# Kernel optimization log

Hardware: AMD Instinct MI355X
Metric: run time of the kernel (lower is better)

Reference implementation:

```python
import jax, jax.numpy as jnp
import numpy as np

LOC_SIZE, CID_SIZE, UID_SIZE, TIM_SIZE = 10000, 300, 1000, 48
LOC_EMB, CID_EMB, UID_EMB, TIM_EMB = 256, 64, 64, 32
HID, ENC_HID = 500, 250            # hidden_size, history_hidden_size
SEQ, TGT = 2048, 256
INPUT = LOC_EMB + TIM_EMB + CID_EMB  # 352


def setup_inputs() -> dict:
    key = jax.random.key(0)
    ks = jax.random.split(key, 32)
    n = lambda i, shape, s=0.05: (jax.random.normal(ks[i], shape, dtype=jnp.float32) * s)
    d = {}
    d["loc"] = jax.random.randint(ks[0], (SEQ, 1), 0, LOC_SIZE)
    d["tim"] = jax.random.randint(ks[1], (SEQ, 1), 0, TIM_SIZE)
    d["cid"] = jax.random.randint(ks[2], (SEQ, 1), 0, CID_SIZE)
    d["uid"] = jax.random.randint(ks[3], (1,), 0, UID_SIZE)
    d["target"] = jax.random.randint(ks[4], (TGT, 1), 0, LOC_SIZE)
    d["target_len"] = TGT
    d["time_sim_matrix"] = jax.random.uniform(ks[5], (TIM_SIZE, TIM_SIZE), dtype=jnp.float32)
    # keep distances away from 0 since the model computes 1/dist
    d["poi_distance_matrix"] = jax.random.uniform(ks[6], (LOC_SIZE, LOC_SIZE), dtype=jnp.float32, minval=0.1, maxval=2.0)
    d["poi_cid_tim"] = jax.random.uniform(ks[7], (TIM_SIZE, CID_SIZE), dtype=jnp.float32)
    # embedding tables (emb_loc/emb_cid are pretrained+frozen in the original)
    d["weight"] = n(8, (LOC_SIZE, LOC_EMB))
    d["weight_cid"] = n(9, (CID_SIZE, CID_EMB))
    d["emb_uid_w"] = n(10, (UID_SIZE, UID_EMB))
    d["emb_tim_w"] = n(11, (TIM_SIZE, TIM_EMB))
    # bidirectional encoder LSTM (hidden 250), gate order i,f,g,o like torch
    d["enc_Wih_f"] = n(12, (4 * ENC_HID, INPUT))
    d["enc_Whh_f"] = n(13, (4 * ENC_HID, ENC_HID))
    d["enc_b_f"] = jnp.zeros((4 * ENC_HID,), jnp.float32)
    d["enc_Wih_b"] = n(14, (4 * ENC_HID, INPUT))
    d["enc_Whh_b"] = n(15, (4 * ENC_HID, ENC_HID))
    d["enc_b_b"] = jnp.zeros((4 * ENC_HID,), jnp.float32)
    # decoder LSTM (hidden 500)
    d["dec_Wih"] = n(16, (4 * HID, INPUT))
    d["dec_Whh"] = n(17, (4 * HID, HID))
    d["dec_b"] = jnp.zeros((4 * HID,), jnp.float32)
    # linear layers
    d["fc_user_w"] = n(18, (HID, UID_EMB))
    d["fc_user_b"] = jnp.zeros((HID,), jnp.float32)
    d["fc_final_w"] = n(19, (LOC_SIZE, 3 * HID))
    d["fc_final_b"] = jnp.zeros((LOC_SIZE,), jnp.float32)
    d["fc_final2_w"] = n(20, (HID, 3 * HID))
    d["fc_final2_b"] = jnp.zeros((HID,), jnp.float32)
    return d


def _lstm(x, Wih, Whh, b, H):
    """Single-layer LSTM, batch=1. x: [T, D] -> hs: [T, H]."""
    h0 = jnp.zeros((H,), x.dtype)
    c0 = jnp.zeros((H,), x.dtype)

    def step(carry, xt):
        h, c = carry
        z = Wih @ xt + Whh @ h + b
        i, f, g, o = jnp.split(z, 4)
        c = jax.nn.sigmoid(f) * c + jax.nn.sigmoid(i) * jnp.tanh(g)
        h = jax.nn.sigmoid(o) * jnp.tanh(c)
        return (h, c), h

    _, hs = jax.lax.scan(step, (h0, c0), x)
    return hs


def _table_attn(history, current, table, invert=False, causal=False):
    """Vectorized replacement for the nested-loop lookup attention.
    energies[i, j] = table[current[i], history[j]] (or its reciprocal),
    upper triangle left at 0 for the self-attn variants (as in the original),
    then softmax over the full row (torch F.softmax default dim=1 on 2D)."""
    e = table[current[:, None], history[None, :]]
    if invert:
        e = 1.0 / e
    if causal:
        nn_ = e.shape[0]
        e = jnp.where(jnp.tril(jnp.ones((nn_, nn_), bool)), e, jnp.zeros((), e.dtype))
    return jax.nn.softmax(e, axis=-1)


def reference(loc, tim, cid, uid, target, target_len,
              time_sim_matrix, poi_distance_matrix, poi_cid_tim,
              weight, weight_cid, emb_uid_w, emb_tim_w,
              enc_Wih_f, enc_Whh_f, enc_b_f, enc_Wih_b, enc_Whh_b, enc_b_b,
              dec_Wih, dec_Whh, dec_b,
              fc_user_w, fc_user_b, fc_final_w, fc_final_b, fc_final2_w, fc_final2_b):
    T = int(target_len)
    loc_f, tim_f, cid_f = loc[:, 0], tim[:, 0], cid[:, 0]

    # cross attention: current window attends to history via lookup tables
    attn_cid_time = _table_attn(cid_f[:-T], tim_f[-T:], poi_cid_tim)
    attn_loc = _table_attn(loc_f[:-T], loc_f[-T:], poi_distance_matrix, invert=True)
    attn_time = _table_attn(tim_f[:-T], tim_f[-T:], time_sim_matrix)
    # self attention on the current window (lower-triangular fill)
    self_cid_time = _table_attn(cid_f[-T:], tim_f[-T:], poi_cid_tim, causal=True)
    self_loc = _table_attn(loc_f[-T:], loc_f[-T:], poi_distance_matrix, invert=True, causal=True)
    self_time = _table_attn(tim_f[-T:], tim_f[-T:], time_sim_matrix, causal=True)

    # embeddings (dropout is identity in eval)
    x = jnp.concatenate([weight[loc_f], emb_tim_w[tim_f], weight_cid[cid_f]], axis=1)  # [SEQ, INPUT]
    hist_x, tgt_x = x[:-T], x[-T:]

    # bidirectional encoder over history
    hf = _lstm(hist_x, enc_Wih_f, enc_Whh_f, enc_b_f, ENC_HID)
    hb = _lstm(hist_x[::-1], enc_Wih_b, enc_Whh_b, enc_b_b, ENC_HID)[::-1]
    hidden_history = jnp.concatenate([hf, hb], axis=1)  # [SEQ-T, 2*ENC_HID=500]

    # decoder over current window
    hidden_state = _lstm(tgt_x, dec_Wih, dec_Whh, dec_b, HID)  # [T, 500]

    target_emb = weight[target[:, 0]]  # [T, LOC_EMB]

    uid_emb = emb_uid_w[uid] @ fc_user_w.T + fc_user_b  # [1, 500]
    user_attn = jax.nn.softmax(uid_emb @ hidden_history.T, axis=-1)  # [1, hist]
    context_user = user_attn @ hidden_history  # [1, 500]

    context = (attn_loc + attn_time + attn_cid_time) @ hidden_history  # [T, 500]
    hidden_state = (self_loc + self_time + self_cid_time) @ hidden_state  # [T, 500]

    hidden_state_all = hidden_state + uid_emb  # broadcast of repeat
    out = jnp.concatenate([hidden_state_all, context,
                           jnp.broadcast_to(context_user, (T, HID))], axis=1)  # [T, 1500]
    y = out @ fc_final_w.T + fc_final_b    # [T, LOC_SIZE]
    y1 = out @ fc_final2_w.T + fc_final2_b  # [T, HID]
    score = jax.nn.log_softmax(y, axis=-1)
    return score, y1, target_emb
```

## Files before the change

### kernel.cpp

```cpp
#include <hip/hip_runtime.h>
#include <stdint.h>

#define HIST 1792
#define TGT 256
#define SEQ 2048
#define INPUT 352
#define EHID 250
#define HID 500

typedef _Float16 h2_t __attribute__((ext_vector_type(2)));

static __device__ __forceinline__ float fdot2(uint32_t a, uint32_t b, float c) {
  return __builtin_amdgcn_fdot2(__builtin_bit_cast(h2_t, a),
                                __builtin_bit_cast(h2_t, b), c, false);
}
static __device__ __forceinline__ uint32_t packh2(float lo, float hi) {
  h2_t h; h[0] = (_Float16)lo; h[1] = (_Float16)hi;
  return __builtin_bit_cast(uint32_t, h);
}
static __device__ __forceinline__ uint4 packq(const float* p) {
  uint4 r;
  r.x = packh2(p[0], p[1]); r.y = packh2(p[2], p[3]);
  r.z = packh2(p[4], p[5]); r.w = packh2(p[6], p[7]);
  return r;
}
static __device__ __forceinline__ float dotq(uint4 w, uint4 h, float acc) {
  acc = fdot2(w.x, h.x, acc); acc = fdot2(w.y, h.y, acc);
  acc = fdot2(w.z, h.z, acc); acc = fdot2(w.w, h.w, acc);
  return acc;
}
static __device__ __forceinline__ float sigf(float x) {
  x = fminf(fmaxf(x, -30.f), 30.f);
  return 1.f / (1.f + __expf(-x));
}
static __device__ __forceinline__ float tanh_f(float x) {
  x = fminf(fmaxf(x, -15.f), 15.f);
  float e = __expf(2.f * x);
  return (e - 1.f) / (e + 1.f);
}
static __device__ __forceinline__ void spin_flag(volatile int* f) {
  while (__hip_atomic_load(f, __ATOMIC_ACQUIRE, __HIP_MEMORY_SCOPE_AGENT) == 0)
    __builtin_amdgcn_s_sleep(2);
}
static __device__ __forceinline__ void spin_cnt(volatile int* f, int target) {
  while (__hip_atomic_load(f, __ATOMIC_ACQUIRE, __HIP_MEMORY_SCOPE_AGENT) < target)
    __builtin_amdgcn_s_sleep(2);
}
#define AW(dst, src) asm("v_accvgpr_write_b32 %0, %1" : "=a"(dst) : "v"(src))
#define AR(dst, src) asm("v_accvgpr_read_b32 %0, %1" : "=v"(dst) : "a"(src))
#define ARQ(dst, arr, base) do { AR(dst.x, arr[(base)+0]); AR(dst.y, arr[(base)+1]); AR(dst.z, arr[(base)+2]); AR(dst.w, arr[(base)+3]); } while(0)

__global__ void k_embed(const int* __restrict__ loc, const int* __restrict__ tim,
                        const int* __restrict__ cid, const int* __restrict__ target,
                        const float* __restrict__ weight, const float* __restrict__ emb_tim_w,
                        const float* __restrict__ weight_cid,
                        float* __restrict__ x, float* __restrict__ te) {
  int t = blockIdx.x, tid = threadIdx.x;
  if (t < SEQ) {
    int l = loc[t], tm = tim[t], cd = cid[t];
    float* xr = x + (size_t)t * INPUT;
    for (int k = tid; k < 256; k += blockDim.x) xr[k] = weight[(size_t)l * 256 + k];
    for (int k = tid; k < 32; k += blockDim.x)  xr[256 + k] = emb_tim_w[tm * 32 + k];
    for (int k = tid; k < 64; k += blockDim.x)  xr[288 + k] = weight_cid[cd * 64 + k];
  } else {
    int i = t - SEQ;
    int tg = target[i];
    for (int k = tid; k < 256; k += blockDim.x) te[(size_t)i * 256 + k] = weight[(size_t)tg * 256 + k];
  }
}

__global__ void k_gemm_t16(const float* __restrict__ A, int lda,
                           const float* __restrict__ W, int ldw,
                           const float* __restrict__ bias,
                           float* __restrict__ C, int ldc,
                           int M, int N, int K, int revA) {
  __shared__ uint32_t AsP[8][65];
  __shared__ uint32_t WsP[8][65];
  const int bn = blockIdx.x * 64, bm = blockIdx.y * 64;
  const int tid = threadIdx.x;
  const int tx = tid & 15, ty = tid >> 4;
  float acc[4][4] = {};
  for (int k0 = 0; k0 < K; k0 += 16) {
    for (int i = tid; i < 512; i += 256) {
      int m = i & 63, kk = i >> 6;
      int gm = bm + m, gk = k0 + 2 * kk;
      float v0 = 0.f, v1 = 0.f;
      if (gm < M) {
        int am = revA ? (M - 1 - gm) : gm;
        if (gk < K)     v0 = A[(size_t)am * lda + gk];
        if (gk + 1 < K) v1 = A[(size_t)am * lda + gk + 1];
      }
      AsP[kk][m] = packh2(v0, v1);
    }
    for (int i = tid; i < 512; i += 256) {
      int n = i & 63, kk = i >> 6;
      int gn = bn + n, gk = k0 + 2 * kk;
      float v0 = 0.f, v1 = 0.f;
      if (gn < N) {
        if (gk < K)     v0 = W[(size_t)gn * ldw + gk];
        if (gk + 1 < K) v1 = W[(size_t)gn * ldw + gk + 1];
      }
      WsP[kk][n] = packh2(v0, v1);
    }
    __syncthreads();
#pragma unroll
    for (int kk = 0; kk < 8; kk++) {
      uint32_t a0 = AsP[kk][ty * 4 + 0], a1 = AsP[kk][ty * 4 + 1], a2 = AsP[kk][ty * 4 + 2], a3 = AsP[kk][ty * 4 + 3];
      uint32_t b0 = WsP[kk][tx * 4 + 0], b1 = WsP[kk][tx * 4 + 1], b2 = WsP[kk][tx * 4 + 2], b3 = WsP[kk][tx * 4 + 3];
      acc[0][0] = fdot2(a0, b0, acc[0][0]); acc[0][1] = fdot2(a0, b1, acc[0][1]);
      acc[0][2] = fdot2(a0, b2, acc[0][2]); acc[0][3] = fdot2(a0, b3, acc[0][3]);
      acc[1][0] = fdot2(a1, b0, acc[1][0]); acc[1][1] = fdot2(a1, b1, acc[1][1]);
      acc[1][2] = fdot2(a1, b2, acc[1][2]); acc[1][3] = fdot2(a1, b3, acc[1][3]);
      acc[2][0] = fdot2(a2, b0, acc[2][0]); acc[2][1] = fdot2(a2, b1, acc[2][1]);
      acc[2][2] = fdot2(a2, b2, acc[2][2]); acc[2][3] = fdot2(a2, b3, acc[2][3]);
      acc[3][0] = fdot2(a3, b0, acc[3][0]); acc[3][1] = fdot2(a3, b1, acc[3][1]);
      acc[3][2] = fdot2(a3, b2, acc[3][2]); acc[3][3] = fdot2(a3, b3, acc[3][3]);
    }
    __syncthreads();
  }
  for (int i = 0; i < 4; i++) {
    int gm = bm + ty * 4 + i; if (gm >= M) continue;
    for (int j = 0; j < 4; j++) {
      int gn = bn + tx * 4 + j; if (gn >= N) continue;
      C[(size_t)gm * ldc + gn] = acc[i][j] + (bias ? bias[gn] : 0.f);
    }
  }
}

__global__ void k_gemm_nn16(const float* __restrict__ A, int lda,
                            const float* __restrict__ B, int ldb,
                            const float* __restrict__ addvec,
                            float* __restrict__ C, int ldc,
                            int M, int N, int K) {
  __shared__ uint32_t AsP[8][65];
  __shared__ uint32_t BsP[8][65];
  const int bn = blockIdx.x * 64, bm = blockIdx.y * 64;
  const int tid = threadIdx.x;
  const int tx = tid & 15, ty = tid >> 4;
  float acc[4][4] = {};
  for (int k0 = 0; k0 < K; k0 += 16) {
    for (int i = tid; i < 512; i += 256) {
      int m = i & 63, kk = i >> 6;
      int gm = bm + m, gk = k0 + 2 * kk;
      float v0 = 0.f, v1 = 0.f;
      if (gm < M) {
        if (gk < K)     v0 = A[(size_t)gm * lda + gk];
        if (gk + 1 < K) v1 = A[(size_t)gm * lda + gk + 1];
      }
      AsP[kk][m] = packh2(v0, v1);
    }
    for (int i = tid; i < 512; i += 256) {
      int n = i & 63, kk = i >> 6;
      int gn = bn + n, gk = k0 + 2 * kk;
      float v0 = 0.f, v1 = 0.f;
      if (gn < N) {
        if (gk < K)     v0 = B[(size_t)gk * ldb + gn];
        if (gk + 1 < K) v1 = B[(size_t)(gk + 1) * ldb + gn];
      }
      BsP[kk][n] = packh2(v0, v1);
    }
    __syncthreads();
#pragma unroll
    for (int kk = 0; kk < 8; kk++) {
      uint32_t a0 = AsP[kk][ty * 4 + 0], a1 = AsP[kk][ty * 4 + 1], a2 = AsP[kk][ty * 4 + 2], a3 = AsP[kk][ty * 4 + 3];
      uint32_t b0 = BsP[kk][tx * 4 + 0], b1 = BsP[kk][tx * 4 + 1], b2 = BsP[kk][tx * 4 + 2], b3 = BsP[kk][tx * 4 + 3];
      acc[0][0] = fdot2(a0, b0, acc[0][0]); acc[0][1] = fdot2(a0, b1, acc[0][1]);
      acc[0][2] = fdot2(a0, b2, acc[0][2]); acc[0][3] = fdot2(a0, b3, acc[0][3]);
      acc[1][0] = fdot2(a1, b0, acc[1][0]); acc[1][1] = fdot2(a1, b1, acc[1][1]);
      acc[1][2] = fdot2(a1, b2, acc[1][2]); acc[1][3] = fdot2(a1, b3, acc[1][3]);
      acc[2][0] = fdot2(a2, b0, acc[2][0]); acc[2][1] = fdot2(a2, b1, acc[2][1]);
      acc[2][2] = fdot2(a2, b2, acc[2][2]); acc[2][3] = fdot2(a2, b3, acc[2][3]);
      acc[3][0] = fdot2(a3, b0, acc[3][0]); acc[3][1] = fdot2(a3, b1, acc[3][1]);
      acc[3][2] = fdot2(a3, b2, acc[3][2]); acc[3][3] = fdot2(a3, b3, acc[3][3]);
    }
    __syncthreads();
  }
  for (int i = 0; i < 4; i++) {
    int gm = bm + ty * 4 + i; if (gm >= M) continue;
    for (int j = 0; j < 4; j++) {
      int gn = bn + tx * 4 + j; if (gn >= N) continue;
      C[(size_t)gm * ldc + gn] = acc[i][j] + (addvec ? addvec[gn] : 0.f);
    }
  }
}

static __device__ void gemm_tile_fused(const float* __restrict__ A, int lda,
                                       const float* __restrict__ W,
                                       const float* __restrict__ bias,
                                       float* __restrict__ C, int ldc,
                                       int M, int N, int bm, int bn, int revA,
                                       int tid, uint32_t* AsP, uint32_t* WsP) {
  const int tx = tid & 15, ty = (tid & 255) >> 4;
  float acc[4][4] = {};
  for (int k0 = 0; k0 < INPUT; k0 += 16) {
    {
      int m = tid & 63, kk = tid >> 6;
      int gm = bm + m, gk = k0 + 2 * kk;
      float v0 = 0.f, v1 = 0.f;
      if (gm < M) {
        int am = revA ? (M - 1 - gm) : gm;
        if (gk < INPUT)     v0 = A[(size_t)am * lda + gk];
        if (gk + 1 < INPUT) v1 = A[(size_t)am * lda + gk + 1];
      }
      AsP[kk * 65 + m] = packh2(v0, v1);
      int gn = bn + m;
      float w0 = 0.f, w1 = 0.f;
      if (gn < N) {
        if (gk < INPUT)     w0 = W[(size_t)gn * INPUT + gk];
        if (gk + 1 < INPUT) w1 = W[(size_t)gn * INPUT + gk + 1];
      }
      WsP[kk * 65 + m] = packh2(w0, w1);
    }
    __syncthreads();
    if (tid < 256) {
#pragma unroll
      for (int kk = 0; kk < 8; kk++) {
        uint32_t a0 = AsP[kk * 65 + ty * 4 + 0], a1 = AsP[kk * 65 + ty * 4 + 1];
        uint32_t a2 = AsP[kk * 65 + ty * 4 + 2], a3 = AsP[kk * 65 + ty * 4 + 3];
        uint32_t b0 = WsP[kk * 65 + tx * 4 + 0], b1 = WsP[kk * 65 + tx * 4 + 1];
        uint32_t b2 = WsP[kk * 65 + tx * 4 + 2], b3 = WsP[kk * 65 + tx * 4 + 3];
        acc[0][0] = fdot2(a0, b0, acc[0][0]); acc[0][1] = fdot2(a0, b1, acc[0][1]);
        acc[0][2] = fdot2(a0, b2, acc[0][2]); acc[0][3] = fdot2(a0, b3, acc[0][3]);
        acc[1][0] = fdot2(a1, b0, acc[1][0]); acc[1][1] = fdot2(a1, b1, acc[1][1]);
        acc[1][2] = fdot2(a1, b2, acc[1][2]); acc[1][3] = fdot2(a1, b3, acc[1][3]);
        acc[2][0] = fdot2(a2, b0, acc[2][0]); acc[2][1] = fdot2(a2, b1, acc[2][1]);
        acc[2][2] = fdot2(a2, b2, acc[2][2]); acc[2][3] = fdot2(a2, b3, acc[2][3]);
        acc[3][0] = fdot2(a3, b0, acc[3][0]); acc[3][1] = fdot2(a3, b1, acc[3][1]);
        acc[3][2] = fdot2(a3, b2, acc[3][2]); acc[3][3] = fdot2(a3, b3, acc[3][3]);
      }
    }
    __syncthreads();
  }
  if (tid < 256) {
    for (int i = 0; i < 4; i++) {
      int gm = bm + ty * 4 + i; if (gm >= M) continue;
      for (int j = 0; j < 4; j++) {
        int gn = bn + tx * 4 + j; if (gn >= N) continue;
        C[(size_t)gm * ldc + gn] = acc[i][j] + bias[gn];
      }
    }
  }
}

#define WQL 12
#define WBYTES (WQL * 512 * 16)
__launch_bounds__(512)
__global__ void k_lstm(const float* __restrict__ x,
                       float* __restrict__ A_f, float* __restrict__ A_b,
                       float* __restrict__ A_d,
                       const float* __restrict__ Wih_f, const float* __restrict__ b_f,
                       const float* __restrict__ Wih_b, const float* __restrict__ b_b,
                       const float* __restrict__ Wih_d, const float* __restrict__ b_d,
                       const float* __restrict__ Whh_f, const float* __restrict__ Whh_b,
                       const float* __restrict__ Whh_d,
                       float* __restrict__ hh, float* __restrict__ hdec,
                       float* zpub, uint32_t* hpub, int* flag_z, int* flag_h, int* cnt,
                       const int* __restrict__ loc, const int* __restrict__ tim,
                       const int* __restrict__ cid,
                       const float* __restrict__ ts, const float* __restrict__ pd,
                       const float* __restrict__ pct,
                       float* __restrict__ S1, float* __restrict__ S2,
                       const int* __restrict__ uid, const float* __restrict__ emb_uid_w,
                       const float* __restrict__ fc_user_w, const float* __restrict__ fc_user_b,
                       float* __restrict__ uid_emb) {
  const int b = blockIdx.x;
  const int tid = threadIdx.x;
  __shared__ __align__(16) unsigned char smem[WBYTES + 2048 + 4096];
  uint4* wl = (uint4*)smem;
  uint4* hbuf = (uint4*)(smem + WBYTES);
  float* zbuf = (float*)(smem + WBYTES + 2048);

  if (b < 6 && tid < 128) hbuf[tid] = make_uint4(0, 0, 0, 0);

  if (b < 2) {
    float* A = (b == 0) ? A_f : A_b;
    const float* Whh = (b == 0) ? Whh_f : Whh_b;
    int* mycnt = cnt + b * 32;
    const bool act = tid < 500;
    uint4 wv0[10], wv1[10];
    uint32_t wa[128];
    if (act) {
      const float* wr0 = Whh + (size_t)tid * EHID;
      const float* wr1 = Whh + (size_t)(tid + 500) * EHID;
#pragma unroll
      for (int q = 0; q < 6; q++) {
        float t0[8], t1[8];
#pragma unroll
        for (int cc = 0; cc < 8; cc++) {
          int col = 208 + 8 * q + cc;
          t0[cc] = (col < EHID) ? wr0[col] : 0.f;
          t1[cc] = (col < EHID) ? wr1[col] : 0.f;
        }
        wl[(q * 2 + 0) * 512 + tid] = packq(t0);
        wl[(q * 2 + 1) * 512 + tid] = packq(t1);
      }
#pragma unroll
      for (int k = 0; k < 16; k++) {
        uint4 p0 = packq(wr0 + 8 * (10 + k));
        uint4 p1 = packq(wr1 + 8 * (10 + k));
        AW(wa[k * 4 + 0], p0.x); AW(wa[k * 4 + 1], p0.y);
        AW(wa[k * 4 + 2], p0.z); AW(wa[k * 4 + 3], p0.w);
        AW(wa[64 + k * 4 + 0], p1.x); AW(wa[64 + k * 4 + 1], p1.y);
        AW(wa[64 + k * 4 + 2], p1.z); AW(wa[64 + k * 4 + 3], p1.w);
      }
#pragma unroll
      for (int q = 0; q < 10; q++) { wv0[q] = packq(wr0 + 8 * q); wv1[q] = packq(wr1 + 8 * q); }
    }
    if (tid == 0) spin_cnt(&mycnt[0], 16);
    __syncthreads();
    float c = 0.f;
    float aA = act ? A[tid] : 0.f;
    float aB = act ? A[500 + tid] : 0.f;
    __syncthreads();
    for (int t = 0; t < HIST; t++) {
      const uint4* hb = hbuf + (t & 1) * 32;
      int tn = (t + 1 < HIST) ? t + 1 : t;
      if ((tn & 63) == 0 && tn > t) {
        if (tid == 0) spin_cnt(&mycnt[tn >> 6], 16);
        __syncthreads();
      }
      if (act) {
        float z0 = aA, z1 = aB, y0 = 0.f, y1 = 0.f;
        aA = A[tn * 1000 + tid];
        aB = A[tn * 1000 + 500 + tid];
#pragma unroll
        for (int q = 0; q < 10; q++) {
          uint4 hq = hb[q];
          z0 = dotq(wv0[q], hq, z0);
          z1 = dotq(wv1[q], hq, z1);
        }
#pragma unroll
        for (int k = 0; k < 16; k++) {
          uint4 hq = hb[10 + k];
          uint4 u0, u1;
          ARQ(u0, wa, k * 4);
          ARQ(u1, wa, 64 + k * 4);
          y0 = dotq(u0, hq, y0);
          y1 = dotq(u1, hq, y1);
        }
#pragma unroll
        for (int q = 0; q < 6; q++) {
          uint4 hq = hb[26 + q];
          z0 = dotq(wl[(q * 2 + 0) * 512 + tid], hq, z0);
          z1 = dotq(wl[(q * 2 + 1) * 512 + tid], hq, z1);
        }
        zbuf[tid] = z0 + y0;
        zbuf[500 + tid] = z1 + y1;
      }
      __syncthreads();
      float hval = 0.f;
      if (tid < EHID) {
        float zi = zbuf[tid], zf = zbuf[250 + tid], zg = zbuf[500 + tid], zo = zbuf[750 + tid];
        c = sigf(zf) * c + sigf(zi) * tanh_f(zg);
        hval = sigf(zo) * tanh_f(c);
        if (b == 0) hh[(size_t)t * HID + tid] = hval;
        else        hh[(size_t)(HIST - 1 - t) * HID + EHID + tid] = hval;
      }
      float hother = __shfl_xor(hval, 1);
      uint32_t* hw = (uint32_t*)(hbuf + ((t + 1) & 1) * 32);
      if (tid < EHID && !(tid & 1)) hw[tid >> 1] = packh2(hval, hother);
      __syncthreads();
    }
  } else if (b < 6) {
    const int gi = b - 2;
    const int j = tid;
    const bool act = (j < 500);
    int* dcnt = cnt + 64;
    uint4 wv[20];
    uint32_t wa[128];
    if (act) {
      const float* wr = Whh_d + (size_t)(gi * 500 + j) * HID;
#pragma unroll
      for (int q = 0; q < 12; q++) {
        float tmp[8];
#pragma unroll
        for (int cc = 0; cc < 8; cc++) {
          int col = 416 + 8 * q + cc;
          tmp[cc] = (col < HID) ? wr[col] : 0.f;
        }
        wl[q * 512 + tid] = packq(tmp);
      }
#pragma unroll
      for (int k = 0; k < 32; k++) {
        uint4 pq = packq(wr + 8 * (20 + k));
        AW(wa[k * 4 + 0], pq.x); AW(wa[k * 4 + 1], pq.y);
        AW(wa[k * 4 + 2], pq.z); AW(wa[k * 4 + 3], pq.w);
      }
#pragma unroll
      for (int q = 0; q < 20; q++) wv[q] = packq(wr + 8 * q);
    }
    if (tid == 0) spin_cnt(&dcnt[0], 32);
    __syncthreads();
    float c = 0.f;
    float aD = act ? A_d[gi * 500 + j] : 0.f;
    __syncthreads();
    for (int t = 0; t < TGT; t++) {
      const uint4* hb = hbuf + (t & 1) * 64;
      int tn = (t + 1 < TGT) ? t + 1 : t;
      if ((tn & 63) == 0 && tn > t) {
        if (tid == 0) spin_cnt(&dcnt[tn >> 6], 32);
        __syncthreads();
      }
      float z = 0.f;
      if (act) {
        float z0 = aD, z1 = 0.f, z2 = 0.f, z3 = 0.f;
        aD = A_d[tn * 2000 + gi * 500 + j];
#pragma unroll
        for (int q = 0; q < 20; q += 2) {
          z0 = dotq(wv[q], hb[q], z0);
          z1 = dotq(wv[q + 1], hb[q + 1], z1);
        }
#pragma unroll
        for (int k = 0; k < 32; k += 2) {
          uint4 u0, u1;
          ARQ(u0, wa, k * 4);
          ARQ(u1, wa, (k + 1) * 4);
          z2 = dotq(u0, hb[20 + k], z2);
          z3 = dotq(u1, hb[21 + k], z3);
        }
#pragma unroll
        for (int q = 0; q < 12; q += 2) {
          z0 = dotq(wl[q * 512 + tid], hb[52 + q], z0);
          z1 = dotq(wl[(q + 1) * 512 + tid], hb[53 + q], z1);
        }
        z = (z0 + z1) + (z2 + z3);
      }
      if (gi < 3) {
        if (act) zpub[gi * 512 + j] = z;
        __threadfence();
        __syncthreads();
        if (tid == 0) {
          __hip_atomic_store(&flag_z[t * 3 + gi], 1, __ATOMIC_RELEASE, __HIP_MEMORY_SCOPE_AGENT);
          spin_flag(&flag_h[t]);
        }
        __syncthreads();
        uint32_t* hw = (uint32_t*)(hbuf + ((t + 1) & 1) * 64);
        if (tid < 250)
          hw[tid] = __hip_atomic_load(&hpub[tid], __ATOMIC_RELAXED, __HIP_MEMORY_SCOPE_AGENT);
        __syncthreads();
      } else {
        if (tid == 0) {
          spin_flag(&flag_z[t * 3 + 0]);
          spin_flag(&flag_z[t * 3 + 1]);
          spin_flag(&flag_z[t * 3 + 2]);
        }
        __syncthreads();
        float hval = 0.f;
        if (act) {
          float zi = __hip_atomic_load(&zpub[0 * 512 + j], __ATOMIC_RELAXED, __HIP_MEMORY_SCOPE_AGENT);
          float zf = __hip_atomic_load(&zpub[1 * 512 + j], __ATOMIC_RELAXED, __HIP_MEMORY_SCOPE_AGENT);
          float zg = __hip_atomic_load(&zpub[2 * 512 + j], __ATOMIC_RELAXED, __HIP_MEMORY_SCOPE_AGENT);
          c = sigf(zf) * c + sigf(zi) * tanh_f(zg);
          hval = sigf(z) * tanh_f(c);
          hdec[(size_t)t * HID + j] = hval;
        }
        float hother = __shfl_xor(hval, 1);
        uint32_t* hw = (uint32_t*)(hbuf + ((t + 1) & 1) * 64);
        if (act && !(j & 1)) {
          uint32_t p = packh2(hval, hother);
          hw[j >> 1] = p;
          __hip_atomic_store(&hpub[j >> 1], p, __ATOMIC_RELAXED, __HIP_MEMORY_SCOPE_AGENT);
        }
        __threadfence();
        __syncthreads();
        if (tid == 0)
          __hip_atomic_store(&flag_h[t], 1, __ATOMIC_RELEASE, __HIP_MEMORY_SCOPE_AGENT);
      }
    }
  } else if (b == 6) {
    float* u = (float*)smem;
    if (tid < 64) u[tid] = emb_uid_w[(size_t)uid[0] * 64 + tid];
    __syncthreads();
    if (tid < HID) {
      float a = fc_user_b[tid];
      for (int k = 0; k < 64; k++) a += u[k] * fc_user_w[tid * 64 + k];
      uid_emb[tid] = a;
    }
  } else if (b < 903) {
    const int g = b - 7;
    const int chunk = g >> 5, w = g & 31;
    uint32_t* AsP = (uint32_t*)smem;
    uint32_t* WsP = AsP + 8 * 65;
    if (w < 16) {
      gemm_tile_fused(x, INPUT, Wih_f, b_f, A_f, 1000, HIST, 1000,
                      chunk * 64, w * 64, 0, tid, AsP, WsP);
      __threadfence();
      __syncthreads();
      if (tid == 0)
        __hip_atomic_fetch_add(&cnt[chunk], 1, __ATOMIC_RELEASE, __HIP_MEMORY_SCOPE_AGENT);
    } else {
      gemm_tile_fused(x, INPUT, Wih_b, b_b, A_b, 1000, HIST, 1000,
                      chunk * 64, (w - 16) * 64, 1, tid, AsP, WsP);
      __threadfence();
      __syncthreads();
      if (tid == 0)
        __hip_atomic_fetch_add(&cnt[32 + chunk], 1, __ATOMIC_RELEASE, __HIP_MEMORY_SCOPE_AGENT);
    }
  } else if (b < 1031) {
    const int g = b - 903;
    const int mt = g >> 5, nt = g & 31;
    uint32_t* AsP = (uint32_t*)smem;
    uint32_t* WsP = AsP + 8 * 65;
    gemm_tile_fused(x + (size_t)HIST * INPUT, INPUT, Wih_d, b_d, A_d, 2000, TGT, 2000,
                    mt * 64, nt * 64, 0, tid, AsP, WsP);
    __threadfence();
    __syncthreads();
    if (tid == 0)
      __hip_atomic_fetch_add(&cnt[64 + mt], 1, __ATOMIC_RELEASE, __HIP_MEMORY_SCOPE_AGENT);
  } else {
    const int i = b - 1031;
    float* e = (float*)smem;
    float* red = ((float*)smem) + HIST;
    const int loc_i = loc[HIST + i], tim_i = tim[HIST + i];
    for (int tab = 0; tab < 3; tab++) {
      for (int jj = tid; jj < HIST; jj += 512) {
        float v;
        if (tab == 0)      v = 1.f / pd[(size_t)loc_i * 10000 + loc[jj]];
        else if (tab == 1) v = ts[tim_i * 48 + tim[jj]];
        else               v = pct[tim_i * 300 + cid[jj]];
        e[jj] = v;
      }
      __syncthreads();
      float mx = -1e30f;
      for (int jj = tid; jj < HIST; jj += 512) mx = fmaxf(mx, e[jj]);
      red[tid] = mx; __syncthreads();
      for (int s = 256; s > 0; s >>= 1) { if (tid < s) red[tid] = fmaxf(red[tid], red[tid + s]); __syncthreads(); }
      mx = red[0]; __syncthreads();
      float sm = 0.f;
      for (int jj = tid; jj < HIST; jj += 512) sm += __expf(e[jj] - mx);
      red[tid] = sm; __syncthreads();
      for (int s = 256; s > 0; s >>= 1) { if (tid < s) red[tid] += red[tid + s]; __syncthreads(); }
      float inv = 1.f / red[0]; __syncthreads();
      for (int jj = tid; jj < HIST; jj += 512) {
        float p = __expf(e[jj] - mx) * inv;
        if (tab == 0) S1[(size_t)i * HIST + jj] = p; else S1[(size_t)i * HIST + jj] += p;
      }
      __syncthreads();
    }
    int lj = 0, tj = 0, cj = 0;
    if (tid < TGT) { lj = loc[HIST + tid]; tj = tim[HIST + tid]; cj = cid[HIST + tid]; }
    for (int tab = 0; tab < 3; tab++) {
      float v = 0.f;
      if (tid < TGT) {
        if (tab == 0)      v = 1.f / pd[(size_t)loc_i * 10000 + lj];
        else if (tab == 1) v = ts[tim_i * 48 + tj];
        else               v = pct[tim_i * 300 + cj];
        if (tid > i) v = 0.f;
        red[tid] = v;
      }
      __syncthreads();
      for (int s = 128; s > 0; s >>= 1) { if (tid < s) red[tid] = fmaxf(red[tid], red[tid + s]); __syncthreads(); }
      float mx = red[0]; __syncthreads();
      float ex = (tid < TGT) ? __expf(v - mx) : 0.f;
      if (tid < TGT) red[tid] = ex;
      __syncthreads();
      for (int s = 128; s > 0; s >>= 1) { if (tid < s) red[tid] += red[tid + s]; __syncthreads(); }
      float p = ex / red[0]; __syncthreads();
      if (tid < TGT) {
        if (tab == 0) S2[(size_t)i * TGT + tid] = p; else S2[(size_t)i * TGT + tid] += p;
      }
      __syncthreads();
    }
  }
}

__global__ void k_user(const float* __restrict__ uid_emb, const float* __restrict__ hh,
                       float* __restrict__ cu) {
  const int tid = threadIdx.x;
  __shared__ float s[HIST];
  __shared__ float red[1024];
  __shared__ __align__(16) float ue[HID];
  if (tid < HID) ue[tid] = uid_emb[tid];
  __syncthreads();
  for (int t = tid; t < HIST; t += 1024) {
    const float4* hr = (const float4*)(hh + (size_t)t * HID);
    const float4* uv = (const float4*)ue;
    float a = 0.f;
#pragma unroll 5
    for (int k = 0; k < 125; k++) {
      float4 h4 = hr[k], u4 = uv[k];
      a += h4.x * u4.x + h4.y * u4.y + h4.z * u4.z + h4.w * u4.w;
    }
    s[t] = a;
  }
  __syncthreads();
  float mx = -1e30f;
  for (int t = tid; t < HIST; t += 1024) mx = fmaxf(mx, s[t]);
  red[tid] = mx; __syncthreads();
  for (int st = 512; st > 0; st >>= 1) { if (tid < st) red[tid] = fmaxf(red[tid], red[tid + st]); __syncthreads(); }
  mx = red[0]; __syncthreads();
  float sm = 0.f;
  for (int t = tid; t < HIST; t += 1024) sm += __expf(s[t] - mx);
  red[tid] = sm; __syncthreads();
  for (int st = 512; st > 0; st >>= 1) { if (tid < st) red[tid] += red[tid + st]; __syncthreads(); }
  float inv = 1.f / red[0]; __syncthreads();
  for (int t = tid; t < HIST; t += 1024) s[t] = __expf(s[t] - mx) * inv;
  __syncthreads();
  if (tid < HID) {
    float a0 = 0.f, a1 = 0.f, a2 = 0.f, a3 = 0.f;
    for (int t = 0; t < HIST; t += 4) {
      a0 += s[t]     * hh[(size_t)t * HID + tid];
      a1 += s[t + 1] * hh[(size_t)(t + 1) * HID + tid];
      a2 += s[t + 2] * hh[(size_t)(t + 2) * HID + tid];
      a3 += s[t + 3] * hh[(size_t)(t + 3) * HID + tid];
    }
    cu[tid] = (a0 + a1) + (a2 + a3);
  }
}

__global__ void k_cubias(const float* __restrict__ cu,
                         const float* __restrict__ Wf, const float* __restrict__ bf,
                         const float* __restrict__ W2, const float* __restrict__ b2,
                         float* __restrict__ fb, float* __restrict__ fb2) {
  __shared__ __align__(16) float cus[HID];
  const int tid = threadIdx.x;
  if (tid < 250) { cus[tid] = cu[tid]; cus[250 + tid] = cu[250 + tid]; }
  __syncthreads();
  int n = blockIdx.x * 256 + tid;
  const float4* cv = (const float4*)cus;
  if (n < 10000) {
    const float4* w = (const float4*)(Wf + (size_t)n * 1500 + 1000);
    float a = bf[n];
#pragma unroll 5
    for (int k = 0; k < 125; k++) {
      float4 wv = w[k], uv = cv[k];
      a += wv.x * uv.x + wv.y * uv.y + wv.z * uv.z + wv.w * uv.w;
    }
    fb[n] = a;
  } else if (n < 10500) {
    int m = n - 10000;
    const float4* w = (const float4*)(W2 + (size_t)m * 1500 + 1000);
    float a = b2[m];
#pragma unroll 5
    for (int k = 0; k < 125; k++) {
      float4 wv = w[k], uv = cv[k];
      a += wv.x * uv.x + wv.y * uv.y + wv.z * uv.z + wv.w * uv.w;
    }
    fb2[m] = a;
  }
}

__global__ void k_logsoftmax(float* __restrict__ y) {
  const int i = blockIdx.x;
  const int tid = threadIdx.x;
  float* r = y + (size_t)i * 10000;
  __shared__ float red[1024];
  float mx = -1e30f;
  for (int j = tid; j < 10000; j += 1024) mx = fmaxf(mx, r[j]);
  red[tid] = mx; __syncthreads();
  for (int s = 512; s > 0; s >>= 1) { if (tid < s) red[tid] = fmaxf(red[tid], red[tid + s]); __syncthreads(); }
  mx = red[0]; __syncthreads();
  float sm = 0.f;
  for (int j = tid; j < 10000; j += 1024) sm += __expf(r[j] - mx);
  red[tid] = sm; __syncthreads();
  for (int s = 512; s > 0; s >>= 1) { if (tid < s) red[tid] += red[tid + s]; __syncthreads(); }
  float lse = mx + __logf(red[0]);
  __syncthreads();
  for (int j = tid; j < 10000; j += 1024) r[j] = r[j] - lse;
}

extern "C" void kernel_launch(void* const* d_in, const int* in_sizes, int n_in,
                              void* d_out, int out_size, void* d_ws, size_t ws_size,
                              hipStream_t stream) {
  (void)in_sizes; (void)n_in; (void)out_size; (void)ws_size;
  const int* loc = (const int*)d_in[0];
  const int* tim = (const int*)d_in[1];
  const int* cid = (const int*)d_in[2];
  const int* uid = (const int*)d_in[3];
  const int* target = (const int*)d_in[4];
  const float* ts = (const float*)d_in[6];
  const float* pd = (const float*)d_in[7];
  const float* pct = (const float*)d_in[8];
  const float* weight = (const float*)d_in[9];
  const float* weight_cid = (const float*)d_in[10];
  const float* emb_uid_w = (const float*)d_in[11];
  const float* emb_tim_w = (const float*)d_in[12];
  const float* enc_Wih_f = (const float*)d_in[13];
  const float* enc_Whh_f = (const float*)d_in[14];
  const float* enc_b_f = (const float*)d_in[15];
  const float* enc_Wih_b = (const float*)d_in[16];
  const float* enc_Whh_b = (const float*)d_in[17];
  const float* enc_b_b = (const float*)d_in[18];
  const float* dec_Wih = (const float*)d_in[19];
  const float* dec_Whh = (const float*)d_in[20];
  const float* dec_b = (const float*)d_in[21];
  const float* fc_user_w = (const float*)d_in[22];
  const float* fc_user_b = (const float*)d_in[23];
  const float* fc_final_w = (const float*)d_in[24];
  const float* fc_final_b = (const float*)d_in[25];
  const float* fc_final2_w = (const float*)d_in[26];
  const float* fc_final2_b = (const float*)d_in[27];

  float* score = (float*)d_out;
  float* y1 = score + (size_t)TGT * 10000;
  float* te = y1 + (size_t)TGT * HID;

  float* ws = (float*)d_ws;
  float* x = ws;
  float* A_f = x + (size_t)SEQ * INPUT;
  float* A_b = A_f + (size_t)HIST * 1000;
  float* A_d = A_b + (size_t)HIST * 1000;
  float* hh = A_d + (size_t)TGT * 2000;
  float* hdec = hh + (size_t)HIST * HID;
  float* S1 = hdec + (size_t)TGT * HID;
  float* S2 = S1 + (size_t)TGT * HIST;
  float* outb = S2 + (size_t)TGT * TGT;
  float* cu = outb + (size_t)TGT * 1000;
  float* fb = cu + 512;
  float* fb2 = fb + 10016;
  float* uid_emb = fb2 + 512;
  float* zpub = uid_emb + 512;
  uint32_t* hpub = (uint32_t*)(zpub + 3 * 512);
  int* flag_z = (int*)(hpub + 256);
  int* flag_h = flag_z + 3 * TGT;
  int* cnt = flag_h + TGT;
  const int n_flags = 4 * TGT + 96;

  k_embed<<<dim3(SEQ + TGT), dim3(128), 0, stream>>>(loc, tim, cid, target, weight, emb_tim_w, weight_cid, x, te);

  hipMemsetAsync(flag_z, 0, n_flags * sizeof(int), stream);

  k_lstm<<<dim3(1287), dim3(512), 0, stream>>>(x, A_f, A_b, A_d,
                                               enc_Wih_f, enc_b_f, enc_Wih_b, enc_b_b,
                                               dec_Wih, dec_b,
                                               enc_Whh_f, enc_Whh_b, dec_Whh,
                                               hh, hdec, zpub, hpub, flag_z, flag_h, cnt,
                                               loc, tim, cid, ts, pd, pct, S1, S2,
                                               uid, emb_uid_w, fc_user_w, fc_user_b, uid_emb);

  k_user<<<dim3(1), dim3(1024), 0, stream>>>(uid_emb, hh, cu);
  k_cubias<<<dim3(42), dim3(256), 0, stream>>>(cu, fc_final_w, fc_final_b,
                                               fc_final2_w, fc_final2_b, fb, fb2);
  k_gemm_nn16<<<dim3(8, 4), dim3(256), 0, stream>>>(S2, TGT, hdec, HID, uid_emb, outb, 1000, TGT, HID, TGT);
  k_gemm_nn16<<<dim3(8, 4), dim3(256), 0, stream>>>(S1, HIST, hh, HID, nullptr, outb + 500, 1000, TGT, HID, HIST);

  k_gemm_t16<<<dim3(157, 4), dim3(256), 0, stream>>>(outb, 1000, fc_final_w, 1500, fb, score, 10000, TGT, 10000, 1000, 0);
  k_gemm_t16<<<dim3(8, 4), dim3(256), 0, stream>>>(outb, 1000, fc_final2_w, 1500, fb2, y1, 500, TGT, 500, 1000, 0);

  k_logsoftmax<<<dim3(TGT), dim3(1024), 0, stream>>>(score);
}
```

Baseline: 4.835 ms.

## Fuse embedding gather into LSTM input GEMM and merge tail kernels

Removes the separate embedding kernel. The LSTM input-projection tiles now gather rows straight from the embedding tables by index, and the target-embedding copy runs as extra blocks of the LSTM kernel. It also merges the user-attention, bias-projection and two attention GEMM kernels into one tail kernel, with a spin flag between the user context and the bias blocks. This saves the intermediate x buffer round trip and several launches, at the cost of indirect loads inside the GEMM loop and a dependency on block co-residency for the spin wait.

```diff
diff --git a/kernel.cpp b/kernel.cpp
--- a/kernel.cpp
+++ b/kernel.cpp
@@ -49,25 +49,6 @@
 #define AW(dst, src) asm("v_accvgpr_write_b32 %0, %1" : "=a"(dst) : "v"(src))
 #define AR(dst, src) asm("v_accvgpr_read_b32 %0, %1" : "=v"(dst) : "a"(src))
 #define ARQ(dst, arr, base) do { AR(dst.x, arr[(base)+0]); AR(dst.y, arr[(base)+1]); AR(dst.z, arr[(base)+2]); AR(dst.w, arr[(base)+3]); } while(0)
-
-__global__ void k_embed(const int* __restrict__ loc, const int* __restrict__ tim,
-                        const int* __restrict__ cid, const int* __restrict__ target,
-                        const float* __restrict__ weight, const float* __restrict__ emb_tim_w,
-                        const float* __restrict__ weight_cid,
-                        float* __restrict__ x, float* __restrict__ te) {
-  int t = blockIdx.x, tid = threadIdx.x;
-  if (t < SEQ) {
-    int l = loc[t], tm = tim[t], cd = cid[t];
-    float* xr = x + (size_t)t * INPUT;
-    for (int k = tid; k < 256; k += blockDim.x) xr[k] = weight[(size_t)l * 256 + k];
-    for (int k = tid; k < 32; k += blockDim.x)  xr[256 + k] = emb_tim_w[tm * 32 + k];
-    for (int k = tid; k < 64; k += blockDim.x)  xr[288 + k] = weight_cid[cd * 64 + k];
-  } else {
-    int i = t - SEQ;
-    int tg = target[i];
-    for (int k = tid; k < 256; k += blockDim.x) te[(size_t)i * 256 + k] = weight[(size_t)tg * 256 + k];
-  }
-}
 
 __global__ void k_gemm_t16(const float* __restrict__ A, int lda,
                            const float* __restrict__ W, int ldw,
@@ -127,69 +108,17 @@
   }
 }
 
-__global__ void k_gemm_nn16(const float* __restrict__ A, int lda,
-                            const float* __restrict__ B, int ldb,
-                            const float* __restrict__ addvec,
-                            float* __restrict__ C, int ldc,
-                            int M, int N, int K) {
-  __shared__ uint32_t AsP[8][65];
-  __shared__ uint32_t BsP[8][65];
-  const int bn = blockIdx.x * 64, bm = blockIdx.y * 64;
-  const int tid = threadIdx.x;
-  const int tx = tid & 15, ty = tid >> 4;
-  float acc[4][4] = {};
-  for (int k0 = 0; k0 < K; k0 += 16) {
-    for (int i = tid; i < 512; i += 256) {
-      int m = i & 63, kk = i >> 6;
-      int gm = bm + m, gk = k0 + 2 * kk;
-      float v0 = 0.f, v1 = 0.f;
-      if (gm < M) {
-        if (gk < K)     v0 = A[(size_t)gm * lda + gk];
-        if (gk + 1 < K) v1 = A[(size_t)gm * lda + gk + 1];
-      }
-      AsP[kk][m] = packh2(v0, v1);
-    }
-    for (int i = tid; i < 512; i += 256) {
-      int n = i & 63, kk = i >> 6;
-      int gn = bn + n, gk = k0 + 2 * kk;
-      float v0 = 0.f, v1 = 0.f;
-      if (gn < N) {
-        if (gk < K)     v0 = B[(size_t)gk * ldb + gn];
-        if (gk + 1 < K) v1 = B[(size_t)(gk + 1) * ldb + gn];
-      }
-      BsP[kk][n] = packh2(v0, v1);
-    }
-    __syncthreads();
-#pragma unroll
-    for (int kk = 0; kk < 8; kk++) {
-      uint32_t a0 = AsP[kk][ty * 4 + 0], a1 = AsP[kk][ty * 4 + 1], a2 = AsP[kk][ty * 4 + 2], a3 = AsP[kk][ty * 4 + 3];
-      uint32_t b0 = BsP[kk][tx * 4 + 0], b1 = BsP[kk][tx * 4 + 1], b2 = BsP[kk][tx * 4 + 2], b3 = BsP[kk][tx * 4 + 3];
-      acc[0][0] = fdot2(a0, b0, acc[0][0]); acc[0][1] = fdot2(a0, b1, acc[0][1]);
-      acc[0][2] = fdot2(a0, b2, acc[0][2]); acc[0][3] = fdot2(a0, b3, acc[0][3]);
-      acc[1][0] = fdot2(a1, b0, acc[1][0]); acc[1][1] = fdot2(a1, b1, acc[1][1]);
-      acc[1][2] = fdot2(a1, b2, acc[1][2]); acc[1][3] = fdot2(a1, b3, acc[1][3]);
-      acc[2][0] = fdot2(a2, b0, acc[2][0]); acc[2][1] = fdot2(a2, b1, acc[2][1]);
-      acc[2][2] = fdot2(a2, b2, acc[2][2]); acc[2][3] = fdot2(a2, b3, acc[2][3]);
-      acc[3][0] = fdot2(a3, b0, acc[3][0]); acc[3][1] = fdot2(a3, b1, acc[3][1]);
-      acc[3][2] = fdot2(a3, b2, acc[3][2]); acc[3][3] = fdot2(a3, b3, acc[3][3]);
-    }
-    __syncthreads();
-  }
-  for (int i = 0; i < 4; i++) {
-    int gm = bm + ty * 4 + i; if (gm >= M) continue;
-    for (int j = 0; j < 4; j++) {
-      int gn = bn + tx * 4 + j; if (gn >= N) continue;
-      C[(size_t)gm * ldc + gn] = acc[i][j] + (addvec ? addvec[gn] : 0.f);
-    }
-  }
-}
-
-static __device__ void gemm_tile_fused(const float* __restrict__ A, int lda,
-                                       const float* __restrict__ W,
-                                       const float* __restrict__ bias,
-                                       float* __restrict__ C, int ldc,
-                                       int M, int N, int bm, int bn, int revA,
-                                       int tid, uint32_t* AsP, uint32_t* WsP) {
+static __device__ void gemm_tile_emb(const int* __restrict__ loc, const int* __restrict__ tim,
+                                     const int* __restrict__ cid,
+                                     const float* __restrict__ weight,
+                                     const float* __restrict__ emb_tim_w,
+                                     const float* __restrict__ weight_cid,
+                                     int rowoff,
+                                     const float* __restrict__ W,
+                                     const float* __restrict__ bias,
+                                     float* __restrict__ C, int ldc,
+                                     int M, int N, int bm, int bn, int revA,
+                                     int tid, uint32_t* AsP, uint32_t* WsP) {
   const int tx = tid & 15, ty = (tid & 255) >> 4;
   float acc[4][4] = {};
   for (int k0 = 0; k0 < INPUT; k0 += 16) {
@@ -198,16 +127,24 @@
       int gm = bm + m, gk = k0 + 2 * kk;
       float v0 = 0.f, v1 = 0.f;
       if (gm < M) {
-        int am = revA ? (M - 1 - gm) : gm;
-        if (gk < INPUT)     v0 = A[(size_t)am * lda + gk];
-        if (gk + 1 < INPUT) v1 = A[(size_t)am * lda + gk + 1];
+        int am = (revA ? (M - 1 - gm) : gm) + rowoff;
+        if (gk < 256) {
+          const float* wp = weight + (size_t)loc[am] * 256 + gk;
+          v0 = wp[0]; v1 = wp[1];
+        } else if (gk < 288) {
+          const float* wp = emb_tim_w + tim[am] * 32 + (gk - 256);
+          v0 = wp[0]; v1 = wp[1];
+        } else {
+          const float* wp = weight_cid + cid[am] * 64 + (gk - 288);
+          v0 = wp[0]; v1 = wp[1];
+        }
       }
       AsP[kk * 65 + m] = packh2(v0, v1);
       int gn = bn + m;
       float w0 = 0.f, w1 = 0.f;
       if (gn < N) {
-        if (gk < INPUT)     w0 = W[(size_t)gn * INPUT + gk];
-        if (gk + 1 < INPUT) w1 = W[(size_t)gn * INPUT + gk + 1];
+        const float* wp = W + (size_t)gn * INPUT + gk;
+        w0 = wp[0]; w1 = wp[1];
       }
       WsP[kk * 65 + m] = packh2(w0, w1);
     }
@@ -242,11 +179,67 @@
   }
 }
 
+static __device__ void nn_tile_fused(const float* __restrict__ A, int lda,
+                                     const float* __restrict__ B, int ldb,
+                                     const float* __restrict__ addvec,
+                                     float* __restrict__ C, int ldc,
+                                     int M, int N, int K, int bm, int bn,
+                                     int tid, uint32_t* AsP, uint32_t* BsP) {
+  const int tx = tid & 15, ty = (tid & 255) >> 4;
+  float acc[4][4] = {};
+  for (int k0 = 0; k0 < K; k0 += 16) {
+    {
+      int m = tid & 63, kk = tid >> 6;
+      int gm = bm + m, gk = k0 + 2 * kk;
+      float v0 = 0.f, v1 = 0.f;
+      if (gm < M) {
+        if (gk < K)     v0 = A[(size_t)gm * lda + gk];
+        if (gk + 1 < K) v1 = A[(size_t)gm * lda + gk + 1];
+      }
+      AsP[kk * 65 + m] = packh2(v0, v1);
+      int gn = bn + m;
+      float w0 = 0.f, w1 = 0.f;
+      if (gn < N) {
+        if (gk < K)     w0 = B[(size_t)gk * ldb + gn];
+        if (gk + 1 < K) w1 = B[(size_t)(gk + 1) * ldb + gn];
+      }
+      BsP[kk * 65 + m] = packh2(w0, w1);
+    }
+    __syncthreads();
+    if (tid < 256) {
+#pragma unroll
+      for (int kk = 0; kk < 8; kk++) {
+        uint32_t a0 = AsP[kk * 65 + ty * 4 + 0], a1 = AsP[kk * 65 + ty * 4 + 1];
+        uint32_t a2 = AsP[kk * 65 + ty * 4 + 2], a3 = AsP[kk * 65 + ty * 4 + 3];
+        uint32_t b0 = BsP[kk * 65 + tx * 4 + 0], b1 = BsP[kk * 65 + tx * 4 + 1];
+        uint32_t b2 = BsP[kk * 65 + tx * 4 + 2], b3 = BsP[kk * 65 + tx * 4 + 3];
+        acc[0][0] = fdot2(a0, b0, acc[0][0]); acc[0][1] = fdot2(a0, b1, acc[0][1]);
+        acc[0][2] = fdot2(a0, b2, acc[0][2]); acc[0][3] = fdot2(a0, b3, acc[0][3]);
+        acc[1][0] = fdot2(a1, b0, acc[1][0]); acc[1][1] = fdot2(a1, b1, acc[1][1]);
+        acc[1][2] = fdot2(a1, b2, acc[1][2]); acc[1][3] = fdot2(a1, b3, acc[1][3]);
+        acc[2][0] = fdot2(a2, b0, acc[2][0]); acc[2][1] = fdot2(a2, b1, acc[2][1]);
+        acc[2][2] = fdot2(a2, b2, acc[2][2]); acc[2][3] = fdot2(a2, b3, acc[2][3]);
+        acc[3][0] = fdot2(a3, b0, acc[3][0]); acc[3][1] = fdot2(a3, b1, acc[3][1]);
+        acc[3][2] = fdot2(a3, b2, acc[3][2]); acc[3][3] = fdot2(a3, b3, acc[3][3]);
+      }
+    }
+    __syncthreads();
+  }
+  if (tid < 256) {
+    for (int i = 0; i < 4; i++) {
+      int gm = bm + ty * 4 + i; if (gm >= M) continue;
+      for (int j = 0; j < 4; j++) {
+        int gn = bn + tx * 4 + j; if (gn >= N) continue;
+        C[(size_t)gm * ldc + gn] = acc[i][j] + (addvec ? addvec[gn] : 0.f);
+      }
+    }
+  }
+}
+
 #define WQL 12
 #define WBYTES (WQL * 512 * 16)
 __launch_bounds__(512)
-__global__ void k_lstm(const float* __restrict__ x,
-                       float* __restrict__ A_f, float* __restrict__ A_b,
+__global__ void k_lstm(float* __restrict__ A_f, float* __restrict__ A_b,
                        float* __restrict__ A_d,
                        const float* __restrict__ Wih_f, const float* __restrict__ b_f,
                        const float* __restrict__ Wih_b, const float* __restrict__ b_b,
@@ -256,13 +249,15 @@
                        float* __restrict__ hh, float* __restrict__ hdec,
                        float* zpub, uint32_t* hpub, int* flag_z, int* flag_h, int* cnt,
                        const int* __restrict__ loc, const int* __restrict__ tim,
-                       const int* __restrict__ cid,
+                       const int* __restrict__ cid, const int* __restrict__ target,
+                       const float* __restrict__ weight, const float* __restrict__ emb_tim_w,
+                       const float* __restrict__ weight_cid,
                        const float* __restrict__ ts, const float* __restrict__ pd,
                        const float* __restrict__ pct,
                        float* __restrict__ S1, float* __restrict__ S2,
                        const int* __restrict__ uid, const float* __restrict__ emb_uid_w,
                        const float* __restrict__ fc_user_w, const float* __restrict__ fc_user_b,
-                       float* __restrict__ uid_emb) {
+                       float* __restrict__ uid_emb, float* __restrict__ te) {
   const int b = blockIdx.x;
   const int tid = threadIdx.x;
   __shared__ __align__(16) unsigned char smem[WBYTES + 2048 + 4096];
@@ -482,15 +477,17 @@
     uint32_t* AsP = (uint32_t*)smem;
     uint32_t* WsP = AsP + 8 * 65;
     if (w < 16) {
-      gemm_tile_fused(x, INPUT, Wih_f, b_f, A_f, 1000, HIST, 1000,
-                      chunk * 64, w * 64, 0, tid, AsP, WsP);
+      gemm_tile_emb(loc, tim, cid, weight, emb_tim_w, weight_cid, 0,
+                    Wih_f, b_f, A_f, 1000, HIST, 1000, chunk * 64, w * 64, 0,
+                    tid, AsP, WsP);
       __threadfence();
       __syncthreads();
       if (tid == 0)
         __hip_atomic_fetch_add(&cnt[chunk], 1, __ATOMIC_RELEASE, __HIP_MEMORY_SCOPE_AGENT);
     } else {
-      gemm_tile_fused(x, INPUT, Wih_b, b_b, A_b, 1000, HIST, 1000,
-                      chunk * 64, (w - 16) * 64, 1, tid, AsP, WsP);
+      gemm_tile_emb(loc, tim, cid, weight, emb_tim_w, weight_cid, 0,
+                    Wih_b, b_b, A_b, 1000, HIST, 1000, chunk * 64, (w - 16) * 64, 1,
+                    tid, AsP, WsP);
       __threadfence();
       __syncthreads();
       if (tid == 0)
@@ -501,13 +498,14 @@
     const int mt = g >> 5, nt = g & 31;
     uint32_t* AsP = (uint32_t*)smem;
     uint32_t* WsP = AsP + 8 * 65;
-    gemm_tile_fused(x + (size_t)HIST * INPUT, INPUT, Wih_d, b_d, A_d, 2000, TGT, 2000,
-                    mt * 64, nt * 64, 0, tid, AsP, WsP);
+    gemm_tile_emb(loc, tim, cid, weight, emb_tim_w, weight_cid, HIST,
+                  Wih_d, b_d, A_d, 2000, TGT, 2000, mt * 64, nt * 64, 0,
+                  tid, AsP, WsP);
     __threadfence();
     __syncthreads();
     if (tid == 0)
       __hip_atomic_fetch_add(&cnt[64 + mt], 1, __ATOMIC_RELEASE, __HIP_MEMORY_SCOPE_AGENT);
-  } else {
+  } else if (b < 1287) {
     const int i = b - 1031;
     float* e = (float*)smem;
     float* red = ((float*)smem) + HIST;
@@ -561,82 +559,112 @@
       }
       __syncthreads();
     }
+  } else {
+    const int r0 = (b - 1287) * 16;
+    for (int idx = tid; idx < 16 * 256; idx += 512) {
+      int row = r0 + (idx >> 8), col = idx & 255;
+      te[(size_t)row * 256 + col] = weight[(size_t)target[row] * 256 + col];
+    }
   }
 }
 
-__global__ void k_user(const float* __restrict__ uid_emb, const float* __restrict__ hh,
-                       float* __restrict__ cu) {
+__launch_bounds__(512)
+__global__ void k_tail(const float* __restrict__ uid_emb, const float* __restrict__ hh,
+                       float* __restrict__ cu, int* cu_flag,
+                       const float* __restrict__ Wf, const float* __restrict__ bf,
+                       const float* __restrict__ W2, const float* __restrict__ b2,
+                       float* __restrict__ fb, float* __restrict__ fb2,
+                       const float* __restrict__ S2, const float* __restrict__ hdec,
+                       const float* __restrict__ S1, float* __restrict__ outb) {
+  const int b = blockIdx.x;
   const int tid = threadIdx.x;
-  __shared__ float s[HIST];
-  __shared__ float red[1024];
-  __shared__ __align__(16) float ue[HID];
-  if (tid < HID) ue[tid] = uid_emb[tid];
-  __syncthreads();
-  for (int t = tid; t < HIST; t += 1024) {
-    const float4* hr = (const float4*)(hh + (size_t)t * HID);
-    const float4* uv = (const float4*)ue;
-    float a = 0.f;
+  __shared__ __align__(16) float sh[HIST + 512];
+  if (b == 0) {
+    float* s = sh;
+    float* red = sh + HIST;
+    __shared__ __align__(16) float ue[HID];
+    if (tid < HID) ue[tid] = uid_emb[tid];
+    __syncthreads();
+    for (int t = tid; t < HIST; t += 512) {
+      const float4* hr = (const float4*)(hh + (size_t)t * HID);
+      const float4* uv = (const float4*)ue;
+      float a = 0.f;
 #pragma unroll 5
-    for (int k = 0; k < 125; k++) {
-      float4 h4 = hr[k], u4 = uv[k];
-      a += h4.x * u4.x + h4.y * u4.y + h4.z * u4.z + h4.w * u4.w;
-    }
-    s[t] = a;
-  }
-  __syncthreads();
-  float mx = -1e30f;
-  for (int t = tid; t < HIST; t += 1024) mx = fmaxf(mx, s[t]);
-  red[tid] = mx; __syncthreads();
-  for (int st = 512; st > 0; st >>= 1) { if (tid < st) red[tid] = fmaxf(red[tid], red[tid + st]); __syncthreads(); }
-  mx = red[0]; __syncthreads();
-  float sm = 0.f;
-  for (int t = tid; t < HIST; t += 1024) sm += __expf(s[t] - mx);
-  red[tid] = sm; __syncthreads();
-  for (int st = 512; st > 0; st >>= 1) { if (tid < st) red[tid] += red[tid + st]; __syncthreads(); }
-  float inv = 1.f / red[0]; __syncthreads();
-  for (int t = tid; t < HIST; t += 1024) s[t] = __expf(s[t] - mx) * inv;
-  __syncthreads();
-  if (tid < HID) {
-    float a0 = 0.f, a1 = 0.f, a2 = 0.f, a3 = 0.f;
-    for (int t = 0; t < HIST; t += 4) {
-      a0 += s[t]     * hh[(size_t)t * HID + tid];
-      a1 += s[t + 1] * hh[(size_t)(t + 1) * HID + tid];
-      a2 += s[t + 2] * hh[(size_t)(t + 2) * HID + tid];
-      a3 += s[t + 3] * hh[(size_t)(t + 3) * HID + tid];
-    }
-    cu[tid] = (a0 + a1) + (a2 + a3);
-  }
-}
-
-__global__ void k_cubias(const float* __restrict__ cu,
-                         const float* __restrict__ Wf, const float* __restrict__ bf,
-                         const float* __restrict__ W2, const float* __restrict__ b2,
-                         float* __restrict__ fb, float* __restrict__ fb2) {
-  __shared__ __align__(16) float cus[HID];
-  const int tid = threadIdx.x;
-  if (tid < 250) { cus[tid] = cu[tid]; cus[250 + tid] = cu[250 + tid]; }
-  __syncthreads();
-  int n = blockIdx.x * 256 + tid;
-  const float4* cv = (const float4*)cus;
-  if (n < 10000) {
-    const float4* w = (const float4*)(Wf + (size_t)n * 1500 + 1000);
-    float a = bf[n];
+      for (int k = 0; k < 125; k++) {
+        float4 h4 = hr[k], u4 = uv[k];
+        a += h4.x * u4.x + h4.y * u4.y + h4.z * u4.z + h4.w * u4.w;
+      }
+      s[t] = a;
+    }
+    __syncthreads();
+    float mx = -1e30f;
+    for (int t = tid; t < HIST; t += 512) mx = fmaxf(mx, s[t]);
+    red[tid] = mx; __syncthreads();
+    for (int st = 256; st > 0; st >>= 1) { if (tid < st) red[tid] = fmaxf(red[tid], red[tid + st]); __syncthreads(); }
+    mx = red[0]; __syncthreads();
+    float sm = 0.f;
+    for (int t = tid; t < HIST; t += 512) sm += __expf(s[t] - mx);
+    red[tid] = sm; __syncthreads();
+    for (int st = 256; st > 0; st >>= 1) { if (tid < st) red[tid] += red[tid + st]; __syncthreads(); }
+    float inv = 1.f / red[0]; __syncthreads();
+    for (int t = tid; t < HIST; t += 512) s[t] = __expf(s[t] - mx) * inv;
+    __syncthreads();
+    if (tid < HID) {
+      float a0 = 0.f, a1 = 0.f, a2 = 0.f, a3 = 0.f;
+      for (int t = 0; t < HIST; t += 4) {
+        a0 += s[t]     * hh[(size_t)t * HID + tid];
+        a1 += s[t + 1] * hh[(size_t)(t + 1) * HID + tid];
+        a2 += s[t + 2] * hh[(size_t)(t + 2) * HID + tid];
+        a3 += s[t + 3] * hh[(size_t)(t + 3) * HID + tid];
+      }
+      cu[tid] = (a0 + a1) + (a2 + a3);
+    }
+    __threadfence();
+    __syncthreads();
+    if (tid == 0)
+      __hip_atomic_store(cu_flag, 1, __ATOMIC_RELEASE, __HIP_MEMORY_SCOPE_AGENT);
+  } else if (b < 22) {
+    float* cus = sh;
+    if (tid == 0) spin_flag(cu_flag);
+    __syncthreads();
+    if (tid < 500) cus[tid] = __hip_atomic_load(&cu[tid], __ATOMIC_RELAXED, __HIP_MEMORY_SCOPE_AGENT);
+    __syncthreads();
+    int n = (b - 1) * 512 + tid;
+    const float4* cv = (const float4*)cus;
+    if (n < 10000) {
+      const float4* w = (const float4*)(Wf + (size_t)n * 1500 + 1000);
+      float a = bf[n];
 #pragma unroll 5
-    for (int k = 0; k < 125; k++) {
-      float4 wv = w[k], uv = cv[k];
-      a += wv.x * uv.x + wv.y * uv.y + wv.z * uv.z + wv.w * uv.w;
-    }
-    fb[n] = a;
-  } else if (n < 10500) {
-    int m = n - 10000;
-    const float4* w = (const float4*)(W2 + (size_t)m * 1500 + 1000);
-    float a = b2[m];
+      for (int k = 0; k < 125; k++) {
+        float4 wv = w[k], uv = cv[k];
+        a += wv.x * uv.x + wv.y * uv.y + wv.z * uv.z + wv.w * uv.w;
+      }
+      fb[n] = a;
+    } else if (n < 10500) {
+      int m = n - 10000;
+      const float4* w = (const float4*)(W2 + (size_t)m * 1500 + 1000);
+      float a = b2[m];
 #pragma unroll 5
-    for (int k = 0; k < 125; k++) {
-      float4 wv = w[k], uv = cv[k];
-      a += wv.x * uv.x + wv.y * uv.y + wv.z * uv.z + wv.w * uv.w;
-    }
-    fb2[m] = a;
+      for (int k = 0; k < 125; k++) {
+        float4 wv = w[k], uv = cv[k];
+        a += wv.x * uv.x + wv.y * uv.y + wv.z * uv.z + wv.w * uv.w;
+      }
+      fb2[m] = a;
+    }
+  } else if (b < 54) {
+    const int g = b - 22;
+    const int nt = g & 7, mt = g >> 3;
+    uint32_t* AsP = (uint32_t*)sh;
+    uint32_t* BsP = AsP + 8 * 65;
+    nn_tile_fused(S2, TGT, hdec, HID, uid_emb, outb, 1000,
+                  TGT, HID, TGT, mt * 64, nt * 64, tid, AsP, BsP);
+  } else {
+    const int g = b - 54;
+    const int nt = g & 7, mt = g >> 3;
+    uint32_t* AsP = (uint32_t*)sh;
+    uint32_t* BsP = AsP + 8 * 65;
+    nn_tile_fused(S1, HIST, hh, HID, nullptr, outb + 500, 1000,
+                  TGT, HID, HIST, mt * 64, nt * 64, tid, AsP, BsP);
   }
 }
 
@@ -696,8 +724,7 @@
   float* te = y1 + (size_t)TGT * HID;
 
   float* ws = (float*)d_ws;
-  float* x = ws;
-  float* A_f = x + (size_t)SEQ * INPUT;
+  float* A_f = ws;
   float* A_b = A_f + (size_t)HIST * 1000;
   float* A_d = A_b + (size_t)HIST * 1000;
   float* hh = A_d + (size_t)TGT * 2000;
@@ -714,25 +741,26 @@
   int* flag_z = (int*)(hpub + 256);
   int* flag_h = flag_z + 3 * TGT;
   int* cnt = flag_h + TGT;
-  const int n_flags = 4 * TGT + 96;
-
-  k_embed<<<dim3(SEQ + TGT), dim3(128), 0, stream>>>(loc, tim, cid, target, weight, emb_tim_w, weight_cid, x, te);
+  int* cu_flag = cnt + 96;
+  const int n_flags = 4 * TGT + 96 + 1;
 
   hipMemsetAsync(flag_z, 0, n_flags * sizeof(int), stream);
 
-  k_lstm<<<dim3(1287), dim3(512), 0, stream>>>(x, A_f, A_b, A_d,
+  k_lstm<<<dim3(1303), dim3(512), 0, stream>>>(A_f, A_b, A_d,
                                                enc_Wih_f, enc_b_f, enc_Wih_b, enc_b_b,
                                                dec_Wih, dec_b,
                                                enc_Whh_f, enc_Whh_b, dec_Whh,
                                                hh, hdec, zpub, hpub, flag_z, flag_h, cnt,
-                                               loc, tim, cid, ts, pd, pct, S1, S2,
-                                               uid, emb_uid_w, fc_user_w, fc_user_b, uid_emb);
-
-  k_user<<<dim3(1), dim3(1024), 0, stream>>>(uid_emb, hh, cu);
-  k_cubias<<<dim3(42), dim3(256), 0, stream>>>(cu, fc_final_w, fc_final_b,
-                                               fc_final2_w, fc_final2_b, fb, fb2);
-  k_gemm_nn16<<<dim3(8, 4), dim3(256), 0, stream>>>(S2, TGT, hdec, HID, uid_emb, outb, 1000, TGT, HID, TGT);
-  k_gemm_nn16<<<dim3(8, 4), dim3(256), 0, stream>>>(S1, HIST, hh, HID, nullptr, outb + 500, 1000, TGT, HID, HIST);
+                                               loc, tim, cid, target,
+                                               weight, emb_tim_w, weight_cid,
+                                               ts, pd, pct, S1, S2,
+                                               uid, emb_uid_w, fc_user_w, fc_user_b,
+                                               uid_emb, te);
+
+  k_tail<<<dim3(86), dim3(512), 0, stream>>>(uid_emb, hh, cu, cu_flag,
+                                             fc_final_w, fc_final_b,
+                                             fc_final2_w, fc_final2_b, fb, fb2,
+                                             S2, hdec, S1, outb);
 
   k_gemm_t16<<<dim3(157, 4), dim3(256), 0, stream>>>(outb, 1000, fc_final_w, 1500, fb, score, 10000, TGT, 10000, 1000, 0);
   k_gemm_t16<<<dim3(8, 4), dim3(256), 0, stream>>>(outb, 1000, fc_final2_w, 1500, fb2, y1, 500, TGT, 500, 1000, 0);
```

New measurement: 4.647 ms. -3.9%, faster.
